# Optimization experiments

Measured on AMD Instinct MI355X. Metric: run time of the kernel, lower is better.

Reference implementation:

```python
import jax, jax.numpy as jnp
from jax import lax
import numpy as np

B = 512
IN_CAPS, OUT_CAPS, IN_DIM, OUT_DIM, ITERS = 32 * 6 * 6, 10, 8, 16, 3
EPS = 1e-8


def setup_inputs() -> dict:
    key = jax.random.key(0)
    ks = jax.random.split(key, 12)
    inp = {
        "x": jax.random.normal(ks[0], (B, 1, 28, 28), dtype=jnp.float32),
        "conv1_w": jax.random.normal(ks[1], (256, 1, 9, 9), dtype=jnp.float32) * 0.05,
        "conv1_b": jnp.zeros((256,), dtype=jnp.float32),
        "conv2_w": jax.random.normal(ks[2], (256, 256, 9, 9), dtype=jnp.float32) * 0.02,
        "conv2_b": jnp.zeros((256,), dtype=jnp.float32),
        "W": jax.random.normal(ks[3], (IN_CAPS, OUT_CAPS, IN_DIM, OUT_DIM), dtype=jnp.float32) * 0.1,
        "d1_w": jax.random.normal(ks[4], (OUT_DIM * OUT_CAPS, 512), dtype=jnp.float32) * 0.05,
        "d1_b": jnp.zeros((512,), dtype=jnp.float32),
        "d2_w": jax.random.normal(ks[5], (512, 1024), dtype=jnp.float32) * 0.05,
        "d2_b": jnp.zeros((1024,), dtype=jnp.float32),
        "d3_w": jax.random.normal(ks[6], (1024, 28 * 28), dtype=jnp.float32) * 0.05,
        "d3_b": jnp.zeros((28 * 28,), dtype=jnp.float32),
    }
    return inp


def _squash(s):
    # s2/(1+s2) * s/sqrt(s2+eps), norm over last dim
    s2 = jnp.sum(s * s, axis=-1, keepdims=True)
    return s2 / (1.0 + s2) * (s / jnp.sqrt(s2 + EPS))


def _conv(x, w, b, stride):
    y = lax.conv_general_dilated(x, w, (stride, stride), "VALID",
                                 dimension_numbers=("NCHW", "OIHW", "NCHW"))
    return y + b[None, :, None, None]


def reference(x, conv1_w, conv1_b, conv2_w, conv2_b, W,
              d1_w, d1_b, d2_w, d2_b, d3_w, d3_b):
    h = jax.nn.relu(_conv(x, conv1_w, conv1_b, 1))          # [B,256,20,20]
    h = _conv(h, conv2_w, conv2_b, 2)                       # [B,256,6,6]
    u = h.reshape(h.shape[0], 8, IN_CAPS).transpose(0, 2, 1)  # [B,1152,8]
    u = _squash(u)

    # dynamic routing
    u_hat = jnp.einsum("ijnm,bin->bijm", W, u)              # [B,1152,10,16]
    b_log = jnp.zeros((u.shape[0], IN_CAPS, OUT_CAPS), dtype=u.dtype)
    v = None
    for _ in range(ITERS):
        c = jax.nn.softmax(b_log, axis=1)                   # over in_capsules (as original)
        s = jnp.einsum("bij,bijm->bjm", c, u_hat)           # [B,10,16]
        v = _squash(s)
        b_log = b_log + jnp.einsum("bjm,bijm->bij", v, u_hat)
    caps = v                                                # [B,10,16]

    pred = jnp.argmax(jnp.sum(caps * caps, axis=-1), axis=-1)  # [B]
    mask = jax.lax.stop_gradient(jax.nn.one_hot(pred, OUT_CAPS, dtype=caps.dtype))
    dec_in = (caps * mask[:, :, None]).reshape(caps.shape[0], -1)  # [B,160]
    r = jax.nn.relu(dec_in @ d1_w + d1_b)
    r = jax.nn.relu(r @ d2_w + d2_b)
    r = jax.nn.sigmoid(r @ d3_w + d3_b)
    recon = r.reshape(-1, 1, 28, 28)
    return caps, recon, pred
```

## Files before the change

kernel.cpp:

```cpp
#include <hip/hip_runtime.h>

#define CAPS_EPS 1e-8f

typedef __attribute__((ext_vector_type(8))) short short8;
typedef __attribute__((ext_vector_type(4))) float f32x4;

__device__ inline ushort bf16_rn(float f) {
    uint u = __float_as_uint(f);
    u += 0x7fff + ((u >> 16) & 1);
    return (ushort)(u >> 16);
}
__device__ inline float bf16_f(ushort h) { return __uint_as_float((uint)h << 16); }

__device__ __forceinline__ void gld16(const void* g, void* l) {
    __builtin_amdgcn_global_load_lds(
        (const __attribute__((address_space(1))) unsigned int*)g,
        (__attribute__((address_space(3))) unsigned int*)l, 16, 0, 0);
}


__global__ __launch_bounds__(256) void k_pre(const float* __restrict__ w2,
                                             ushort* __restrict__ wBhi,
                                             ushort* __restrict__ wBlo,
                                             const float* __restrict__ x,
                                             ushort* __restrict__ xhi,
                                             ushort* __restrict__ xlo,
                                             const float* __restrict__ w1,
                                             ushort* __restrict__ w1phi,
                                             ushort* __restrict__ w1plo) {
    int bx = blockIdx.x, tid = threadIdx.x;
    if (bx < 256) {
        __shared__ float ld[81 * 65];
        int n = bx;
        const float* src = w2 + (size_t)n * 20736;
        for (int cc = 0; cc < 4; ++cc) {
            for (int i = tid; i < 5184; i += 256) {
                int c_loc = i / 81, t = i - c_loc * 81;
                ld[t * 65 + c_loc] = src[cc * 5184 + i];
            }
            __syncthreads();
            for (int i = tid; i < 5184; i += 256) {
                int t = i >> 6, c_loc = i & 63;
                float f = ld[t * 65 + c_loc];
                ushort hi = bf16_rn(f);
                ushort lo = bf16_rn(f - bf16_f(hi));
                size_t o = (size_t)n * 20736 + t * 256 + cc * 64 + c_loc;
                wBhi[o] = hi;
                wBlo[o] = lo;
            }
            __syncthreads();
        }
    } else if (bx < 256 + 1569) {
        int idx = (bx - 256) * 256 + tid;
        if (idx < 401408) {
            float f = x[idx];
            ushort hi = bf16_rn(f);
            ushort lo = bf16_rn(f - bf16_f(hi));
            xhi[idx] = hi;
            xlo[idx] = lo;
        } else if (idx < 401472) {
            xhi[idx] = 0;
            xlo[idx] = 0;
        }
    } else {
        int idx = (bx - 1825) * 256 + tid;
        int c = idx / 160;
        int kk160 = idx - c * 160;
        int kstep = kk160 >> 5, kk = kk160 & 31;
        int ky = kstep * 2 + (kk >> 4), kx = kk & 15;
        float f = (ky < 9 && kx < 9) ? w1[c * 81 + ky * 9 + kx] : 0.f;
        ushort hi = bf16_rn(f);
        ushort lo = bf16_rn(f - bf16_f(hi));
        w1phi[idx] = hi;
        w1plo[idx] = lo;
    }
}

__global__ __launch_bounds__(256) void k_conv1m(const ushort* __restrict__ xhi,
                                                const ushort* __restrict__ xlo,
                                                const ushort* __restrict__ w1phi,
                                                const ushort* __restrict__ w1plo,
                                                const float* __restrict__ b1,
                                                ushort* __restrict__ h1hi,
                                                ushort* __restrict__ h1lo) {
    int tid = threadIdx.x;
    int wv = tid >> 6, lane = tid & 63;
    int lrow = lane & 15, quad = lane >> 4;
    int m0 = blockIdx.x * 128 + wv * 32;
    int c0 = blockIdx.y * 64;

    int am[2];
#pragma unroll
    for (int t = 0; t < 2; ++t) {
        int m = m0 + t * 16 + lrow;
        int b = m / 400, r = m - b * 400;
        int y = r / 20, xx = r - y * 20;
        am[t] = b * 784 + y * 28 + xx;
    }

    f32x4 acc[2][4];
#pragma unroll
    for (int t = 0; t < 2; ++t)
#pragma unroll
        for (int tn = 0; tn < 4; ++tn) acc[t][tn] = (f32x4){0.f, 0.f, 0.f, 0.f};

    for (int kstep = 0; kstep < 5; ++kstep) {
        int arow = (kstep * 2 + (quad >> 1)) * 28 + (quad & 1) * 8;
        int boff = kstep * 32 + quad * 8;
        short8 bh[4], bl2[4];
#pragma unroll
        for (int tn = 0; tn < 4; ++tn) {
            int br = (c0 + tn * 16 + lrow) * 160 + boff;
            bh[tn] = *reinterpret_cast<const short8*>(w1phi + br);
            bl2[tn] = *reinterpret_cast<const short8*>(w1plo + br);
        }
#pragma unroll
        for (int t = 0; t < 2; ++t) {
            short8 ah = *reinterpret_cast<const short8*>(xhi + am[t] + arow);
            short8 al = *reinterpret_cast<const short8*>(xlo + am[t] + arow);
#pragma unroll
            for (int tn = 0; tn < 4; ++tn) {
                acc[t][tn] = __builtin_amdgcn_mfma_f32_16x16x32_bf16(ah, bh[tn], acc[t][tn], 0, 0, 0);
                acc[t][tn] = __builtin_amdgcn_mfma_f32_16x16x32_bf16(ah, bl2[tn], acc[t][tn], 0, 0, 0);
                acc[t][tn] = __builtin_amdgcn_mfma_f32_16x16x32_bf16(al, bh[tn], acc[t][tn], 0, 0, 0);
            }
        }
    }

#pragma unroll
    for (int t = 0; t < 2; ++t)
#pragma unroll
        for (int r = 0; r < 4; ++r) {
            int m = m0 + t * 16 + quad * 4 + r;
#pragma unroll
            for (int tn = 0; tn < 4; ++tn) {
                int c = c0 + tn * 16 + lrow;
                float v = acc[t][tn][r] + b1[c];
                v = fmaxf(v, 0.f);
                ushort hi = bf16_rn(v);
                ushort lo = bf16_rn(v - bf16_f(hi));
                h1hi[(size_t)m * 256 + c] = hi;
                h1lo[(size_t)m * 256 + c] = lo;
            }
        }
}

__global__ __launch_bounds__(256) void k_h2init4(const float* __restrict__ b2,
                                                 float* __restrict__ h2) {
    size_t idx = (size_t)blockIdx.x * 256 + threadIdx.x;
    const float4* b24 = reinterpret_cast<const float4*>(b2);
    reinterpret_cast<float4*>(h2)[idx] = b24[idx & 63];
}

__global__ __launch_bounds__(256, 2) void k_conv2m(const ushort* __restrict__ h1hi,
                                                   const ushort* __restrict__ h1lo,
                                                   const ushort* __restrict__ wBhi,
                                                   const ushort* __restrict__ wBlo,
                                                   float* __restrict__ h2) {
    __shared__ ushort Ahi[128 * 32];
    __shared__ ushort Alo[128 * 32];
    __shared__ ushort Bhi[256 * 32];
    __shared__ ushort Blo[256 * 32];
    int tid = threadIdx.x;
    int m0 = blockIdx.x * 128;
    int kbase = blockIdx.y * 2592;

    int wv = tid >> 6, lane = tid & 63;
    int cq = (lane & 3) * 8;

    int ra = wv * 32 + (lane >> 2);
    int mA0 = m0 + ra, mA1 = mA0 + 16;
    int mb0 = mA0 / 36, mp0 = mA0 - mb0 * 36;
    int mb1 = mA1 / 36, mp1 = mA1 - mb1 * 36;
    size_t a0 = ((size_t)mb0 * 400 + (mp0 / 6) * 40 + (mp0 % 6) * 2) * 256 + cq;
    size_t a1 = ((size_t)mb1 * 400 + (mp1 / 6) * 40 + (mp1 % 6) * 2) * 256 + cq;
    int ldsA = wv * 1024;

    int rb = wv * 64 + (lane >> 2);
    size_t bB = (size_t)rb * 20736 + cq;
    int ldsB = wv * 2048;

    int mhalf = (wv >> 1) * 64, nhalf = (wv & 1) * 128;
    int lrow = lane & 15, quad = lane >> 4;

    f32x4 acc[4][8];
#pragma unroll
    for (int a = 0; a < 4; ++a)
#pragma unroll
        for (int bq = 0; bq < 8; ++bq) acc[a][bq] = (f32x4){0.f, 0.f, 0.f, 0.f};

    for (int ks = 0; ks < 81; ++ks) {
        int k = kbase + ks * 32;
        int t = k >> 8, cc = k & 255;
        int ky = t / 9, kx = t - ky * 9;
        size_t koffA = (size_t)(ky * 5120 + kx * 256 + cc);

        __syncthreads();
        gld16(h1hi + a0 + koffA, &Ahi[ldsA]);
        gld16(h1hi + a1 + koffA, &Ahi[ldsA + 512]);
        gld16(h1lo + a0 + koffA, &Alo[ldsA]);
        gld16(h1lo + a1 + koffA, &Alo[ldsA + 512]);
#pragma unroll
        for (int q = 0; q < 4; ++q) {
            size_t bo = bB + (size_t)q * 331776 + k;
            gld16(wBhi + bo, &Bhi[ldsB + q * 512]);
            gld16(wBlo + bo, &Blo[ldsB + q * 512]);
        }
        __syncthreads();

        short8 ah[4], al[4];
#pragma unroll
        for (int tm = 0; tm < 4; ++tm) {
            int off = (mhalf + tm * 16 + lrow) * 32 + quad * 8;
            ah[tm] = *reinterpret_cast<short8*>(&Ahi[off]);
            al[tm] = *reinterpret_cast<short8*>(&Alo[off]);
        }
#pragma unroll
        for (int tn = 0; tn < 8; ++tn) {
            int off = (nhalf + tn * 16 + lrow) * 32 + quad * 8;
            short8 bh = *reinterpret_cast<short8*>(&Bhi[off]);
            short8 bl2 = *reinterpret_cast<short8*>(&Blo[off]);
#pragma unroll
            for (int tm = 0; tm < 4; ++tm) {
                acc[tm][tn] = __builtin_amdgcn_mfma_f32_16x16x32_bf16(ah[tm], bh, acc[tm][tn], 0, 0, 0);
                acc[tm][tn] = __builtin_amdgcn_mfma_f32_16x16x32_bf16(ah[tm], bl2, acc[tm][tn], 0, 0, 0);
                acc[tm][tn] = __builtin_amdgcn_mfma_f32_16x16x32_bf16(al[tm], bh, acc[tm][tn], 0, 0, 0);
            }
        }
    }

#pragma unroll
    for (int tm = 0; tm < 4; ++tm) {
        int mrow = m0 + mhalf + tm * 16 + quad * 4;
#pragma unroll
        for (int tn = 0; tn < 8; ++tn) {
            int ncol = nhalf + tn * 16 + lrow;
#pragma unroll
            for (int r = 0; r < 4; ++r)
                atomicAdd(&h2[(size_t)(mrow + r) * 256 + ncol], acc[tm][tn][r]);
        }
    }
}

__device__ __forceinline__ void wtrans(const float* __restrict__ src,
                                       ushort* __restrict__ dh,
                                       ushort* __restrict__ dl,
                                       float* ld, int kt, int nt, int K, int N,
                                       int tid) {
    for (int i = tid; i < 4096; i += 256) {
        int kk = i >> 6, nn = i & 63;
        int k = kt * 64 + kk, n = nt * 64 + nn;
        float f = (k < K && n < N) ? src[(size_t)k * N + n] : 0.f;
        ld[kk * 65 + nn] = f;
    }
    __syncthreads();
    for (int i = tid; i < 4096; i += 256) {
        int nn = i >> 6, kk = i & 63;
        int k = kt * 64 + kk, n = nt * 64 + nn;
        if (k < K) {
            float f = ld[kk * 65 + nn];
            ushort hi = bf16_rn(f);
            ushort lo = bf16_rn(f - bf16_f(hi));
            dh[(size_t)n * K + k] = hi;
            dl[(size_t)n * K + k] = lo;
        }
    }
}

__global__ __launch_bounds__(256) void k_post(const float* __restrict__ h2,
                                              float* __restrict__ uT,
                                              float* __restrict__ zr,
                                              const float* __restrict__ d1w,
                                              const float* __restrict__ d2w,
                                              const float* __restrict__ d3w,
                                              ushort* __restrict__ d1wThi, ushort* __restrict__ d1wTlo,
                                              ushort* __restrict__ d2wThi, ushort* __restrict__ d2wTlo,
                                              ushort* __restrict__ d3wThi, ushort* __restrict__ d3wTlo) {
    __shared__ float smem[8224 + 1056];
    int bx = blockIdx.x, t = threadIdx.x;
    if (bx < 576) {
        float (*ld)[257] = (float (*)[257])smem;
        float (*scl)[33] = (float (*)[33])(smem + 8224);
        int s = bx % 36;
        int b0 = (bx / 36) * 32;
        for (int bb = 0; bb < 32; ++bb)
            ld[bb][t] = h2[((size_t)(b0 + bb) * 36 + s) * 256 + t];
        __syncthreads();
        int b = t & 31, gb = (t >> 5) * 4;
#pragma unroll
        for (int q = 0; q < 4; ++q) {
            int g = gb + q;
            float s2 = 0.f;
#pragma unroll
            for (int n = 0; n < 8; ++n) {
                float vv = ld[b][g + n * 32];
                s2 = fmaf(vv, vv, s2);
            }
            scl[b][g] = s2 / ((1.f + s2) * sqrtf(s2 + CAPS_EPS));
        }
        __syncthreads();
        int hf = t >> 5;
        for (int gg = 0; gg < 32; ++gg) {
            int idx = hf * 32 + gg;
            int g = idx >> 3, n = idx & 7;
            uT[(((size_t)g * 36 + s) * 8 + n) * 512 + b0 + b] = ld[b][g + n * 32] * scl[b][g];
        }
    } else if (bx < 6421) {
        reinterpret_cast<float4*>(zr)[(size_t)(bx - 576) * 256 + t] = make_float4(0, 0, 0, 0);
    } else if (bx < 6445) {
        int local = bx - 6421;
        wtrans(d1w, d1wThi, d1wTlo, smem, local / 8, local % 8, 160, 512, t);
    } else if (bx < 6573) {
        int local = bx - 6445;
        wtrans(d2w, d2wThi, d2wTlo, smem, local / 16, local % 16, 512, 1024, t);
    } else {
        int local = bx - 6573;
        wtrans(d3w, d3wThi, d3wTlo, smem, local / 14, local % 14, 1024, 784, t);
    }
}

__global__ __launch_bounds__(256) void k_s(const float* __restrict__ Wc,
                                           const float* __restrict__ uT,
                                           const float* __restrict__ bl,
                                           float* __restrict__ sT,
                                           int first) {
    __shared__ float lw[8 * 1280];
    int tid = threadIdx.x;
    int i0 = blockIdx.x * 8;
    int b = blockIdx.y * 128 + (tid & 127);
    int mh = tid >> 7;
    const float* wg = Wc + (size_t)i0 * 1280;
#pragma unroll
    for (int r = 0; r < 10; ++r) {
        int q4 = (r * 256 + tid) * 4;
        *reinterpret_cast<float4*>(&lw[q4]) = *reinterpret_cast<const float4*>(wg + q4);
    }
    __syncthreads();
    float acc[80];
#pragma unroll
    for (int q = 0; q < 80; ++q) acc[q] = 0.f;
    for (int di = 0; di < 8; ++di) {
        int i = i0 + di;
        float ur[8];
#pragma unroll
        for (int n = 0; n < 8; ++n) ur[n] = uT[((size_t)i * 8 + n) * 512 + b];
#pragma unroll
        for (int j = 0; j < 10; ++j) {
            float c;
            if (first) c = 1.0f;
            else c = expf(bl[((size_t)i * 10 + j) * 512 + b]);
            const float* wp = &lw[(di * 10 + j) * 128 + mh * 8];
            float4 s0 = {0.f, 0.f, 0.f, 0.f}, s1 = {0.f, 0.f, 0.f, 0.f};
#pragma unroll
            for (int n = 0; n < 8; ++n) {
                const float4* wq = reinterpret_cast<const float4*>(wp + n * 16);
                float4 wa = wq[0], wb = wq[1];
                float un = ur[n];
                s0.x = fmaf(un, wa.x, s0.x); s0.y = fmaf(un, wa.y, s0.y);
                s0.z = fmaf(un, wa.z, s0.z); s0.w = fmaf(un, wa.w, s0.w);
                s1.x = fmaf(un, wb.x, s1.x); s1.y = fmaf(un, wb.y, s1.y);
                s1.z = fmaf(un, wb.z, s1.z); s1.w = fmaf(un, wb.w, s1.w);
            }
            acc[j * 8 + 0] = fmaf(c, s0.x, acc[j * 8 + 0]);
            acc[j * 8 + 1] = fmaf(c, s0.y, acc[j * 8 + 1]);
            acc[j * 8 + 2] = fmaf(c, s0.z, acc[j * 8 + 2]);
            acc[j * 8 + 3] = fmaf(c, s0.w, acc[j * 8 + 3]);
            acc[j * 8 + 4] = fmaf(c, s1.x, acc[j * 8 + 4]);
            acc[j * 8 + 5] = fmaf(c, s1.y, acc[j * 8 + 5]);
            acc[j * 8 + 6] = fmaf(c, s1.z, acc[j * 8 + 6]);
            acc[j * 8 + 7] = fmaf(c, s1.w, acc[j * 8 + 7]);
        }
    }
#pragma unroll
    for (int j = 0; j < 10; ++j)
#pragma unroll
        for (int mm = 0; mm < 8; ++mm)
            atomicAdd(&sT[(j * 16 + mh * 8 + mm) * 512 + b], acc[j * 8 + mm]);
}

__global__ __launch_bounds__(256) void k_v(const float* __restrict__ sT,
                                           const float* __restrict__ Z,
                                           float* __restrict__ v,
                                           float* __restrict__ vT,
                                           float* __restrict__ sTz,
                                           float* __restrict__ Zz,
                                           int first) {
    int idx = blockIdx.x * 256 + threadIdx.x;
    int j = idx >> 9;
    int b = idx & 511;
    float rz = first ? (1.0f / 1152.0f) : (1.0f / Z[j * 512 + b]);
    float sv[16];
    float s2 = 0.f;
#pragma unroll
    for (int m = 0; m < 16; ++m) {
        sv[m] = sT[(j * 16 + m) * 512 + b] * rz;
        s2 = fmaf(sv[m], sv[m], s2);
    }
    float scale = s2 / ((1.f + s2) * sqrtf(s2 + CAPS_EPS));
#pragma unroll
    for (int m = 0; m < 16; ++m) {
        float val = sv[m] * scale;
        v[(size_t)b * 160 + j * 16 + m] = val;
        vT[(j * 16 + m) * 512 + b] = val;
        sTz[(j * 16 + m) * 512 + b] = 0.f;
    }
    Zz[idx] = 0.f;
}

__global__ __launch_bounds__(256) void k_bupd(const float* __restrict__ Wc,
                                              const float* __restrict__ uT,
                                              const float* __restrict__ vT,
                                              float* __restrict__ bl,
                                              float* __restrict__ Z) {
    __shared__ float lw[8 * 1280];
    int tid = threadIdx.x;
    int i0 = blockIdx.x * 8;
    int b = blockIdx.y * 128 + (tid & 127);
    int ih = tid >> 7;
    const float* wg = Wc + (size_t)i0 * 1280;
#pragma unroll
    for (int r = 0; r < 10; ++r) {
        int q4 = (r * 256 + tid) * 4;
        *reinterpret_cast<float4*>(&lw[q4]) = *reinterpret_cast<const float4*>(wg + q4);
    }
    __syncthreads();
    float ur[4][8];
#pragma unroll
    for (int ii = 0; ii < 4; ++ii) {
        int i = i0 + ih * 4 + ii;
#pragma unroll
        for (int n = 0; n < 8; ++n) ur[ii][n] = uT[((size_t)i * 8 + n) * 512 + b];
    }
    for (int j = 0; j < 10; ++j) {
        float vj[16];
#pragma unroll
        for (int m = 0; m < 16; ++m) vj[m] = vT[(j * 16 + m) * 512 + b];
        float zp = 0.f;
#pragma unroll
        for (int ii = 0; ii < 4; ++ii) {
            int di = ih * 4 + ii;
            const float* wp = &lw[(di * 10 + j) * 128];
            float t = 0.f;
#pragma unroll
            for (int n = 0; n < 8; ++n) {
                const float4* wq = reinterpret_cast<const float4*>(wp + n * 16);
                float4 w0 = wq[0], w1 = wq[1], w2 = wq[2], w3 = wq[3];
                float wvv = w0.x * vj[0];
                wvv = fmaf(w0.y, vj[1], wvv);  wvv = fmaf(w0.z, vj[2], wvv);
                wvv = fmaf(w0.w, vj[3], wvv);  wvv = fmaf(w1.x, vj[4], wvv);
                wvv = fmaf(w1.y, vj[5], wvv);  wvv = fmaf(w1.z, vj[6], wvv);
                wvv = fmaf(w1.w, vj[7], wvv);  wvv = fmaf(w2.x, vj[8], wvv);
                wvv = fmaf(w2.y, vj[9], wvv);  wvv = fmaf(w2.z, vj[10], wvv);
                wvv = fmaf(w2.w, vj[11], wvv); wvv = fmaf(w3.x, vj[12], wvv);
                wvv = fmaf(w3.y, vj[13], wvv); wvv = fmaf(w3.z, vj[14], wvv);
                wvv = fmaf(w3.w, vj[15], wvv);
                t = fmaf(ur[ii][n], wvv, t);
            }
            size_t idx = ((size_t)(i0 + di) * 10 + j) * 512 + b;
            float nb = bl[idx] + t;
            bl[idx] = nb;
            zp += expf(nb);
        }
        atomicAdd(&Z[j * 512 + b], zp);
    }
}

__global__ __launch_bounds__(256) void k_predv(const float* __restrict__ sT,
                                               const float* __restrict__ Z,
                                               float* __restrict__ out,
                                               ushort* __restrict__ dechi,
                                               ushort* __restrict__ declo,
                                               int pred_off) {
    int b = blockIdx.x, t = threadIdx.x;
    __shared__ float sq[160];
    __shared__ float scl[10];
    __shared__ float vnrm[10];
    __shared__ int ip;
    float raw = 0.f;
    int j = t >> 4;
    if (t < 160) {
        raw = sT[(size_t)t * 512 + b] / Z[j * 512 + b];
        sq[t] = raw * raw;
    }
    __syncthreads();
    if (t < 10) {
        float s = 0.f;
#pragma unroll
        for (int k = 0; k < 16; ++k) s += sq[t * 16 + k];
        float sc = s / ((1.f + s) * sqrtf(s + CAPS_EPS));
        scl[t] = sc;
        vnrm[t] = s * sc * sc;
    }
    __syncthreads();
    float val = 0.f;
    if (t < 160) {
        val = raw * scl[j];
        out[(size_t)b * 160 + t] = val;
    }
    if (t == 0) {
        float best = vnrm[0];
        int bi = 0;
        for (int jj = 1; jj < 10; ++jj)
            if (vnrm[jj] > best) { best = vnrm[jj]; bi = jj; }
        ip = bi;
        out[(size_t)pred_off + b] = (float)bi;
    }
    __syncthreads();
    if (t < 160) {
        float d = (j == ip) ? val : 0.f;
        ushort hi = bf16_rn(d);
        ushort lo = bf16_rn(d - bf16_f(hi));
        dechi[(size_t)b * 160 + t] = hi;
        declo[(size_t)b * 160 + t] = lo;
    }
}

template <int ACT, int SPLIT_OUT>
__global__ __launch_bounds__(256) void k_gemmm(const ushort* __restrict__ Ahi,
                                               const ushort* __restrict__ Alo,
                                               const ushort* __restrict__ Bhi,
                                               const ushort* __restrict__ Blo,
                                               const float* __restrict__ bias,
                                               ushort* __restrict__ Chi,
                                               ushort* __restrict__ Clo,
                                               float* __restrict__ Cf,
                                               int K, int Ng) {
    int tid = threadIdx.x;
    int wv = tid >> 6, lane = tid & 63;
    int lrow = lane & 15, quad = lane >> 4;
    int m0 = blockIdx.x * 64 + (wv >> 1) * 32;
    int n0 = blockIdx.y * 128 + (wv & 1) * 64;

    f32x4 acc[2][4];
#pragma unroll
    for (int t = 0; t < 2; ++t)
#pragma unroll
        for (int tn = 0; tn < 4; ++tn) acc[t][tn] = (f32x4){0.f, 0.f, 0.f, 0.f};

    for (int ks = 0; ks < K; ks += 32) {
        int boff = ks + quad * 8;
        short8 bh[4], bl2[4];
#pragma unroll
        for (int tn = 0; tn < 4; ++tn) {
            size_t br = (size_t)(n0 + tn * 16 + lrow) * K + boff;
            bh[tn] = *reinterpret_cast<const short8*>(Bhi + br);
            bl2[tn] = *reinterpret_cast<const short8*>(Blo + br);
        }
#pragma unroll
        for (int t = 0; t < 2; ++t) {
            size_t ar = (size_t)(m0 + t * 16 + lrow) * K + boff;
            short8 ah = *reinterpret_cast<const short8*>(Ahi + ar);
            short8 al = *reinterpret_cast<const short8*>(Alo + ar);
#pragma unroll
            for (int tn = 0; tn < 4; ++tn) {
                acc[t][tn] = __builtin_amdgcn_mfma_f32_16x16x32_bf16(ah, bh[tn], acc[t][tn], 0, 0, 0);
                acc[t][tn] = __builtin_amdgcn_mfma_f32_16x16x32_bf16(ah, bl2[tn], acc[t][tn], 0, 0, 0);
                acc[t][tn] = __builtin_amdgcn_mfma_f32_16x16x32_bf16(al, bh[tn], acc[t][tn], 0, 0, 0);
            }
        }
    }

#pragma unroll
    for (int t = 0; t < 2; ++t)
#pragma unroll
        for (int r = 0; r < 4; ++r) {
            int m = m0 + t * 16 + quad * 4 + r;
#pragma unroll
            for (int tn = 0; tn < 4; ++tn) {
                int n = n0 + tn * 16 + lrow;
                if (n < Ng) {
                    float val = acc[t][tn][r] + bias[n];
                    if (ACT == 0) val = fmaxf(val, 0.f);
                    else val = 1.f / (1.f + expf(-val));
                    if (SPLIT_OUT) {
                        ushort hi = bf16_rn(val);
                        ushort lo = bf16_rn(val - bf16_f(hi));
                        Chi[(size_t)m * Ng + n] = hi;
                        Clo[(size_t)m * Ng + n] = lo;
                    } else {
                        Cf[(size_t)m * Ng + n] = val;
                    }
                }
            }
        }
}

extern "C" void kernel_launch(void* const* d_in, const int* in_sizes, int n_in,
                              void* d_out, int out_size, void* d_ws, size_t ws_size,
                              hipStream_t stream) {
    const float* x   = (const float*)d_in[0];
    const float* w1  = (const float*)d_in[1];
    const float* b1  = (const float*)d_in[2];
    const float* w2  = (const float*)d_in[3];
    const float* b2  = (const float*)d_in[4];
    const float* Wc  = (const float*)d_in[5];
    const float* d1w = (const float*)d_in[6];
    const float* d1b = (const float*)d_in[7];
    const float* d2w = (const float*)d_in[8];
    const float* d2b = (const float*)d_in[9];
    const float* d3w = (const float*)d_in[10];
    const float* d3b = (const float*)d_in[11];
    float* out = (float*)d_out;

    ushort* wBhi = (ushort*)d_ws;
    ushort* wBlo = wBhi + 5308416;
    ushort* h1hi = (ushort*)((char*)d_ws + 21233664);
    ushort* h1lo = h1hi + 52428800;
    char*   h2b  = (char*)d_ws + 230948864;
    float*  h2   = (float*)h2b;
    ushort* xhi   = (ushort*)h2b;
    ushort* xlo   = xhi + 401472;
    ushort* w1phi = xlo + 401472;
    ushort* w1plo = w1phi + 40960;

    float* post = (float*)((char*)d_ws + 21233664);
    float* uT  = post + 4718592;
    float* bl  = post + 9437184;
    float* sT  = post + 15335424;
    float* Z   = post + 15417344;
    float* v   = post + 15422464;
    float* vT  = post + 15504384;
    ushort* ub = (ushort*)(post + 15586304);
    ushort* dechi   = ub;
    ushort* declo   = ub + 81920;
    ushort* r1hi    = ub + 163840;
    ushort* r1lo    = ub + 425984;
    ushort* r2hi    = ub + 688128;
    ushort* r2lo    = ub + 1212416;
    ushort* d1wThi  = ub + 1736704;
    ushort* d1wTlo  = ub + 1818624;
    ushort* d2wThi  = ub + 1900544;
    ushort* d2wTlo  = ub + 2424832;
    ushort* d3wThi  = ub + 2949120;
    ushort* d3wTlo  = ub + 3866624;

    int pred_off = out_size - 512;

    k_pre<<<1985, 256, 0, stream>>>(w2, wBhi, wBlo, x, xhi, xlo, w1, w1phi, w1plo);
    k_conv1m<<<dim3(1600, 4), 256, 0, stream>>>(xhi, xlo, w1phi, w1plo, b1, h1hi, h1lo);
    k_h2init4<<<4608, 256, 0, stream>>>(b2, h2);
    k_conv2m<<<dim3(144, 8), 256, 0, stream>>>(h1hi, h1lo, wBhi, wBlo, h2);
    k_post<<<6797, 256, 0, stream>>>(h2, uT, bl, d1w, d2w, d3w,
                                     d1wThi, d1wTlo, d2wThi, d2wTlo, d3wThi, d3wTlo);

    k_s<<<dim3(144, 4), 256, 0, stream>>>(Wc, uT, bl, sT, 1);
    k_v<<<20, 256, 0, stream>>>(sT, Z, v, vT, sT, Z, 1);
    k_bupd<<<dim3(144, 4), 256, 0, stream>>>(Wc, uT, vT, bl, Z);
    k_s<<<dim3(144, 4), 256, 0, stream>>>(Wc, uT, bl, sT, 0);
    k_v<<<20, 256, 0, stream>>>(sT, Z, v, vT, sT, Z, 0);
    k_bupd<<<dim3(144, 4), 256, 0, stream>>>(Wc, uT, vT, bl, Z);
    k_s<<<dim3(144, 4), 256, 0, stream>>>(Wc, uT, bl, sT, 0);
    k_predv<<<512, 256, 0, stream>>>(sT, Z, out, dechi, declo, pred_off);

    k_gemmm<0, 1><<<dim3(8, 4), 256, 0, stream>>>(dechi, declo, d1wThi, d1wTlo, d1b,
                                                  r1hi, r1lo, nullptr, 160, 512);
    k_gemmm<0, 1><<<dim3(8, 8), 256, 0, stream>>>(r1hi, r1lo, d2wThi, d2wTlo, d2b,
                                                  r2hi, r2lo, nullptr, 512, 1024);
    k_gemmm<1, 0><<<dim3(8, 7), 256, 0, stream>>>(r2hi, r2lo, d3wThi, d3wTlo, d3b,
                                                  nullptr, nullptr, out + 81920, 1024, 784);
}
```

Measured before the change: 1.344 ms.

## Fuse squash into routing update, fold conv2 bias into post, split weight prep

```diff
diff --git a/kernel.cpp b/kernel.cpp
--- a/kernel.cpp
+++ b/kernel.cpp
@@ -29,29 +29,26 @@
                                              ushort* __restrict__ w1phi,
                                              ushort* __restrict__ w1plo) {
     int bx = blockIdx.x, tid = threadIdx.x;
-    if (bx < 256) {
+    if (bx < 1024) {
         __shared__ float ld[81 * 65];
-        int n = bx;
-        const float* src = w2 + (size_t)n * 20736;
-        for (int cc = 0; cc < 4; ++cc) {
-            for (int i = tid; i < 5184; i += 256) {
-                int c_loc = i / 81, t = i - c_loc * 81;
-                ld[t * 65 + c_loc] = src[cc * 5184 + i];
-            }
-            __syncthreads();
-            for (int i = tid; i < 5184; i += 256) {
-                int t = i >> 6, c_loc = i & 63;
-                float f = ld[t * 65 + c_loc];
-                ushort hi = bf16_rn(f);
-                ushort lo = bf16_rn(f - bf16_f(hi));
-                size_t o = (size_t)n * 20736 + t * 256 + cc * 64 + c_loc;
-                wBhi[o] = hi;
-                wBlo[o] = lo;
-            }
-            __syncthreads();
-        }
-    } else if (bx < 256 + 1569) {
-        int idx = (bx - 256) * 256 + tid;
+        int n = bx >> 2, cc = bx & 3;
+        const float* src = w2 + (size_t)n * 20736 + cc * 5184;
+        for (int i = tid; i < 5184; i += 256) {
+            int c_loc = i / 81, t = i - c_loc * 81;
+            ld[t * 65 + c_loc] = src[i];
+        }
+        __syncthreads();
+        for (int i = tid; i < 5184; i += 256) {
+            int t = i >> 6, c_loc = i & 63;
+            float f = ld[t * 65 + c_loc];
+            ushort hi = bf16_rn(f);
+            ushort lo = bf16_rn(f - bf16_f(hi));
+            size_t o = (size_t)n * 20736 + t * 256 + cc * 64 + c_loc;
+            wBhi[o] = hi;
+            wBlo[o] = lo;
+        }
+    } else if (bx < 1024 + 1569) {
+        int idx = (bx - 1024) * 256 + tid;
         if (idx < 401408) {
             float f = x[idx];
             ushort hi = bf16_rn(f);
@@ -63,7 +60,7 @@
             xlo[idx] = 0;
         }
     } else {
-        int idx = (bx - 1825) * 256 + tid;
+        int idx = (bx - 2593) * 256 + tid;
         int c = idx / 160;
         int kk160 = idx - c * 160;
         int kstep = kk160 >> 5, kk = kk160 & 31;
@@ -145,13 +142,6 @@
         }
 }
 
-__global__ __launch_bounds__(256) void k_h2init4(const float* __restrict__ b2,
-                                                 float* __restrict__ h2) {
-    size_t idx = (size_t)blockIdx.x * 256 + threadIdx.x;
-    const float4* b24 = reinterpret_cast<const float4*>(b2);
-    reinterpret_cast<float4*>(h2)[idx] = b24[idx & 63];
-}
-
 __global__ __launch_bounds__(256, 2) void k_conv2m(const ushort* __restrict__ h1hi,
                                                    const ushort* __restrict__ h1lo,
                                                    const ushort* __restrict__ wBhi,
@@ -268,6 +258,7 @@
 }
 
 __global__ __launch_bounds__(256) void k_post(const float* __restrict__ h2,
+                                              const float* __restrict__ b2,
                                               float* __restrict__ uT,
                                               float* __restrict__ zr,
                                               const float* __restrict__ d1w,
@@ -283,8 +274,9 @@
         float (*scl)[33] = (float (*)[33])(smem + 8224);
         int s = bx % 36;
         int b0 = (bx / 36) * 32;
+        float bias = b2[t];
         for (int bb = 0; bb < 32; ++bb)
-            ld[bb][t] = h2[((size_t)(b0 + bb) * 36 + s) * 256 + t];
+            ld[bb][t] = h2[((size_t)(b0 + bb) * 36 + s) * 256 + t] + bias;
         __syncthreads();
         int b = t & 31, gb = (t >> 5) * 4;
 #pragma unroll
@@ -305,16 +297,16 @@
             int g = idx >> 3, n = idx & 7;
             uT[(((size_t)g * 36 + s) * 8 + n) * 512 + b0 + b] = ld[b][g + n * 32] * scl[b][g];
         }
-    } else if (bx < 6421) {
+    } else if (bx < 6506) {
         reinterpret_cast<float4*>(zr)[(size_t)(bx - 576) * 256 + t] = make_float4(0, 0, 0, 0);
-    } else if (bx < 6445) {
-        int local = bx - 6421;
+    } else if (bx < 6530) {
+        int local = bx - 6506;
         wtrans(d1w, d1wThi, d1wTlo, smem, local / 8, local % 8, 160, 512, t);
-    } else if (bx < 6573) {
-        int local = bx - 6445;
+    } else if (bx < 6658) {
+        int local = bx - 6530;
         wtrans(d2w, d2wThi, d2wTlo, smem, local / 16, local % 16, 512, 1024, t);
     } else {
-        int local = bx - 6573;
+        int local = bx - 6658;
         wtrans(d3w, d3wThi, d3wTlo, smem, local / 14, local % 14, 1024, 784, t);
     }
 }
@@ -323,12 +315,20 @@
                                            const float* __restrict__ uT,
                                            const float* __restrict__ bl,
                                            float* __restrict__ sT,
+                                           float* __restrict__ Znext,
                                            int first) {
     __shared__ float lw[8 * 1280];
     int tid = threadIdx.x;
     int i0 = blockIdx.x * 8;
-    int b = blockIdx.y * 128 + (tid & 127);
+    int bg = blockIdx.y;
+    int b = bg * 128 + (tid & 127);
     int mh = tid >> 7;
+    if (blockIdx.x == 0) {
+        for (int q = tid; q < 1280; q += 256) {
+            int j = q >> 7, bb = q & 127;
+            Znext[j * 512 + bg * 128 + bb] = 0.f;
+        }
+    }
     const float* wg = Wc + (size_t)i0 * 1280;
 #pragma unroll
     for (int r = 0; r < 10; ++r) {
@@ -378,45 +378,26 @@
             atomicAdd(&sT[(j * 16 + mh * 8 + mm) * 512 + b], acc[j * 8 + mm]);
 }
 
-__global__ __launch_bounds__(256) void k_v(const float* __restrict__ sT,
-                                           const float* __restrict__ Z,
-                                           float* __restrict__ v,
-                                           float* __restrict__ vT,
-                                           float* __restrict__ sTz,
-                                           float* __restrict__ Zz,
-                                           int first) {
-    int idx = blockIdx.x * 256 + threadIdx.x;
-    int j = idx >> 9;
-    int b = idx & 511;
-    float rz = first ? (1.0f / 1152.0f) : (1.0f / Z[j * 512 + b]);
-    float sv[16];
-    float s2 = 0.f;
-#pragma unroll
-    for (int m = 0; m < 16; ++m) {
-        sv[m] = sT[(j * 16 + m) * 512 + b] * rz;
-        s2 = fmaf(sv[m], sv[m], s2);
-    }
-    float scale = s2 / ((1.f + s2) * sqrtf(s2 + CAPS_EPS));
-#pragma unroll
-    for (int m = 0; m < 16; ++m) {
-        float val = sv[m] * scale;
-        v[(size_t)b * 160 + j * 16 + m] = val;
-        vT[(j * 16 + m) * 512 + b] = val;
-        sTz[(j * 16 + m) * 512 + b] = 0.f;
-    }
-    Zz[idx] = 0.f;
-}
-
 __global__ __launch_bounds__(256) void k_bupd(const float* __restrict__ Wc,
                                               const float* __restrict__ uT,
-                                              const float* __restrict__ vT,
+                                              const float* __restrict__ sTr,
+                                              const float* __restrict__ Zr,
                                               float* __restrict__ bl,
-                                              float* __restrict__ Z) {
+                                              float* __restrict__ Zw,
+                                              float* __restrict__ sTz,
+                                              int first) {
     __shared__ float lw[8 * 1280];
     int tid = threadIdx.x;
     int i0 = blockIdx.x * 8;
-    int b = blockIdx.y * 128 + (tid & 127);
+    int bg = blockIdx.y;
+    int b = bg * 128 + (tid & 127);
     int ih = tid >> 7;
+    if (blockIdx.x == 0) {
+        for (int q = tid; q < 20480; q += 256) {
+            int mq = q >> 7, bb = q & 127;
+            sTz[mq * 512 + bg * 128 + bb] = 0.f;
+        }
+    }
     const float* wg = Wc + (size_t)i0 * 1280;
 #pragma unroll
     for (int r = 0; r < 10; ++r) {
@@ -432,9 +413,19 @@
         for (int n = 0; n < 8; ++n) ur[ii][n] = uT[((size_t)i * 8 + n) * 512 + b];
     }
     for (int j = 0; j < 10; ++j) {
+        float rz = first ? (1.0f / 1152.0f) : (1.0f / Zr[j * 512 + b]);
         float vj[16];
-#pragma unroll
-        for (int m = 0; m < 16; ++m) vj[m] = vT[(j * 16 + m) * 512 + b];
+        float s2 = 0.f;
+#pragma unroll
+        for (int m = 0; m < 16; ++m) {
+            float sv = sTr[(j * 16 + m) * 512 + b] * rz;
+            vj[m] = sv;
+            s2 = fmaf(sv, sv, s2);
+        }
+        float scale = s2 / ((1.f + s2) * sqrtf(s2 + CAPS_EPS));
+#pragma unroll
+        for (int m = 0; m < 16; ++m) vj[m] *= scale;
+
         float zp = 0.f;
 #pragma unroll
         for (int ii = 0; ii < 4; ++ii) {
@@ -456,12 +447,12 @@
                 wvv = fmaf(w3.w, vj[15], wvv);
                 t = fmaf(ur[ii][n], wvv, t);
             }
-            size_t idx = ((size_t)(i0 + di) * 10 + j) * 512 + b;
+            size_t idx = ((size_t)(i0 + ih * 4 + ii) * 10 + j) * 512 + b;
             float nb = bl[idx] + t;
             bl[idx] = nb;
             zp += expf(nb);
         }
-        atomicAdd(&Z[j * 512 + b], zp);
+        atomicAdd(&Zw[j * 512 + b], zp);
     }
 }
 
@@ -616,11 +607,11 @@
     float* post = (float*)((char*)d_ws + 21233664);
     float* uT  = post + 4718592;
     float* bl  = post + 9437184;
-    float* sT  = post + 15335424;
-    float* Z   = post + 15417344;
-    float* v   = post + 15422464;
-    float* vT  = post + 15504384;
-    ushort* ub = (ushort*)(post + 15586304);
+    float* sT0 = post + 15335424;
+    float* sT1 = post + 15417344;
+    float* Z0  = post + 15499264;
+    float* Z1  = post + 15504384;
+    ushort* ub = (ushort*)(post + 15509504);
     ushort* dechi   = ub;
     ushort* declo   = ub + 81920;
     ushort* r1hi    = ub + 163840;
@@ -636,21 +627,19 @@
 
     int pred_off = out_size - 512;
 
-    k_pre<<<1985, 256, 0, stream>>>(w2, wBhi, wBlo, x, xhi, xlo, w1, w1phi, w1plo);
+    k_pre<<<2753, 256, 0, stream>>>(w2, wBhi, wBlo, x, xhi, xlo, w1, w1phi, w1plo);
     k_conv1m<<<dim3(1600, 4), 256, 0, stream>>>(xhi, xlo, w1phi, w1plo, b1, h1hi, h1lo);
-    k_h2init4<<<4608, 256, 0, stream>>>(b2, h2);
+    hipMemsetAsync(h2, 0, 18874368, stream);
     k_conv2m<<<dim3(144, 8), 256, 0, stream>>>(h1hi, h1lo, wBhi, wBlo, h2);
-    k_post<<<6797, 256, 0, stream>>>(h2, uT, bl, d1w, d2w, d3w,
+    k_post<<<6882, 256, 0, stream>>>(h2, b2, uT, bl, d1w, d2w, d3w,
                                      d1wThi, d1wTlo, d2wThi, d2wTlo, d3wThi, d3wTlo);
 
-    k_s<<<dim3(144, 4), 256, 0, stream>>>(Wc, uT, bl, sT, 1);
-    k_v<<<20, 256, 0, stream>>>(sT, Z, v, vT, sT, Z, 1);
-    k_bupd<<<dim3(144, 4), 256, 0, stream>>>(Wc, uT, vT, bl, Z);
-    k_s<<<dim3(144, 4), 256, 0, stream>>>(Wc, uT, bl, sT, 0);
-    k_v<<<20, 256, 0, stream>>>(sT, Z, v, vT, sT, Z, 0);
-    k_bupd<<<dim3(144, 4), 256, 0, stream>>>(Wc, uT, vT, bl, Z);
-    k_s<<<dim3(144, 4), 256, 0, stream>>>(Wc, uT, bl, sT, 0);
-    k_predv<<<512, 256, 0, stream>>>(sT, Z, out, dechi, declo, pred_off);
+    k_s<<<dim3(144, 4), 256, 0, stream>>>(Wc, uT, bl, sT0, Z0, 1);
+    k_bupd<<<dim3(144, 4), 256, 0, stream>>>(Wc, uT, sT0, Z0, bl, Z0, sT1, 1);
+    k_s<<<dim3(144, 4), 256, 0, stream>>>(Wc, uT, bl, sT1, Z1, 0);
+    k_bupd<<<dim3(144, 4), 256, 0, stream>>>(Wc, uT, sT1, Z0, bl, Z1, sT0, 0);
+    k_s<<<dim3(144, 4), 256, 0, stream>>>(Wc, uT, bl, sT0, Z0, 0);
+    k_predv<<<512, 256, 0, stream>>>(sT0, Z1, out, dechi, declo, pred_off);
 
     k_gemmm<0, 1><<<dim3(8, 4), 256, 0, stream>>>(dechi, declo, d1wThi, d1wTlo, d1b,
                                                   r1hi, r1lo, nullptr, 160, 512);
```

Result: slower. 2.133 ms (+58.7%).
